# Kernel optimization log

Hardware: AMD Instinct MI355X
Metric: run time of the kernel (lower is better)

Reference implementation:

```python
import jax, jax.numpy as jnp
import numpy as np


def setup_inputs() -> dict:
    key = jax.random.key(0)
    ks = jax.random.split(key, 7)
    N, E, F_in, H = 50000, 800000, 256, 128
    x = jax.random.normal(ks[0], (N, F_in), dtype=jnp.float32)
    edge_index = jax.random.randint(ks[1], (2, E), 0, N, dtype=jnp.int64)
    edge_weight = jax.random.uniform(ks[2], (E,), dtype=jnp.float32)
    W = jax.random.normal(ks[3], (H, F_in), dtype=jnp.float32) * 0.05
    b = jax.random.normal(ks[4], (H,), dtype=jnp.float32) * 0.05
    W_lin = jax.random.normal(ks[5], (2, H), dtype=jnp.float32) * 0.05
    b_lin = jax.random.normal(ks[6], (2,), dtype=jnp.float32) * 0.05
    return {"x": x, "edge_index": edge_index, "edge_weight": edge_weight,
            "W": W, "b": b, "W_lin": W_lin, "b_lin": b_lin}


def reference(x, edge_index, edge_weight, W, b, W_lin, b_lin):
    # GCNConv (PyG semantics): add self-loops (weight 1), symmetric gcn_norm,
    # linear transform, scatter-add aggregation at target, + bias.
    N = x.shape[0]
    loop = jnp.arange(N, dtype=edge_index.dtype)
    src = jnp.concatenate([edge_index[0], loop])  # [E+N]
    dst = jnp.concatenate([edge_index[1], loop])  # [E+N]
    w = jnp.concatenate([edge_weight, jnp.ones((N,), x.dtype)])  # [E+N]
    deg = jax.ops.segment_sum(w, dst, num_segments=N)  # [N]
    dinv = jnp.where(deg > 0, jax.lax.rsqrt(deg), 0.0)
    norm = dinv[src] * w * dinv[dst]  # [E+N]
    xw = x @ W.T  # [N, H] transform-then-gather (fewer FLOPs than gather-then-transform)
    msg = xw[src] * norm[:, None]  # [E+N, H]
    h = jax.ops.segment_sum(msg, dst, num_segments=N) + b  # [N, H]
    # dropout is identity in eval mode
    h = jax.nn.relu(h)
    out = h @ W_lin.T + b_lin  # [N, 2]
    return jax.nn.sigmoid(out)
```

## Files before the change

kernel.cpp:

```cpp
#include <hip/hip_runtime.h>

#define F_IN 256
#define H_DIM 128
#define BIN 64
#define CAP 2048
#define CH 4096

typedef short bf16x8 __attribute__((ext_vector_type(8)));
typedef float f32x4 __attribute__((ext_vector_type(4)));
typedef unsigned short ushort8 __attribute__((ext_vector_type(8)));

__device__ inline unsigned short f2bf(float f) {
    unsigned int u = __float_as_uint(f);
    u += 0x7fffu + ((u >> 16) & 1u);
    return (unsigned short)(u >> 16);
}
__device__ inline float bf_lo(unsigned int u) { return __uint_as_float(u << 16); }
__device__ inline float bf_hi(unsigned int u) { return __uint_as_float(u & 0xffff0000u); }
__device__ inline unsigned int wfx(int wbits) {
    return (unsigned int)__float2uint_rn(__int_as_float(wbits) * 65536.0f);
}

__global__ __launch_bounds__(256) void zero_cur_kernel(int* __restrict__ gcur, int nbins) {
    int i = blockIdx.x * blockDim.x + threadIdx.x;
    if (i < nbins) gcur[i] = 0;
}

__global__ __launch_bounds__(256) void bin_scatter_kernel(const int* __restrict__ ei,
                                                          const float* __restrict__ ew,
                                                          int* __restrict__ gcur,
                                                          int2* __restrict__ binned,
                                                          int E, int nbins) {
    __shared__ unsigned int bh[1024];
    __shared__ int bb[1024];
    __shared__ unsigned int bc[1024];
    int t = threadIdx.x, blk = blockIdx.x;
    for (int i = t; i < 1024; i += 256) { bh[i] = 0; bc[i] = 0; }
    __syncthreads();
    int e0 = blk * CH, e1 = min(e0 + CH, E);
    for (int i = e0 + t; i < e1; i += 256) atomicAdd(&bh[ei[(size_t)E + i] >> 6], 1u);
    __syncthreads();
    for (int b = t; b < nbins; b += 256) {
        int c = (int)bh[b];
        bb[b] = c ? atomicAdd(&gcur[b], c) : 0;
    }
    __syncthreads();
    for (int i = e0 + t; i < e1; i += 256) {
        int s = ei[i];
        int d = ei[(size_t)E + i];
        float wv = ew[i];
        int bin = d >> 6;
        int r = bb[bin] + (int)atomicAdd(&bc[bin], 1u);
        if (r < CAP) {
            int2 p;
            p.x = s | ((d & 63) << 16);
            p.y = __float_as_int(wv);
            binned[(size_t)bin * CAP + r] = p;
        }
    }
}

__global__ __launch_bounds__(256) void gemm_mfma_kernel(const float* __restrict__ x,
                                                        const float* __restrict__ W,
                                                        const int2* __restrict__ binned,
                                                        const int* __restrict__ gcur,
                                                        unsigned short* __restrict__ xs, int N) {
    __shared__ unsigned short As[64 * 64];
    __shared__ unsigned short Bs[128 * 64];
    __shared__ unsigned int fxg[64];
    __shared__ float sdinv[64];
    const int tid = threadIdx.x;
    const int wv = tid >> 6, lane = tid & 63;
    const int block_row = blockIdx.x * 64;

    if (tid < 64) fxg[tid] = 0;
    __syncthreads();
    {
        int ecnt = min(gcur[blockIdx.x], CAP);
        size_t ebase = (size_t)blockIdx.x * CAP;
        for (int i = tid; i < ecnt; i += 256) {
            int2 p = binned[ebase + i];
            atomicAdd(&fxg[(p.x >> 16) & 63], wfx(p.y));
        }
    }
    __syncthreads();
    if (tid < 64) sdinv[tid] = rsqrtf((float)fxg[tid] * (1.0f / 65536.0f) + 1.0f);

    f32x4 acc[8] = {};

    for (int ks = 0; ks < 4; ks++) {
#pragma unroll
        for (int it = 0; it < 2; it++) {
            int gg = it * 256 + tid;
            int row = gg >> 3, g = gg & 7;
            int gr = block_row + row;
            float4 v0 = {0, 0, 0, 0}, v1 = {0, 0, 0, 0};
            if (gr < N) {
                const float4* p = (const float4*)&x[(size_t)gr * F_IN + ks * 64 + g * 8];
                v0 = p[0]; v1 = p[1];
            }
            ushort8 o;
            o[0] = f2bf(v0.x); o[1] = f2bf(v0.y); o[2] = f2bf(v0.z); o[3] = f2bf(v0.w);
            o[4] = f2bf(v1.x); o[5] = f2bf(v1.y); o[6] = f2bf(v1.z); o[7] = f2bf(v1.w);
            int slot = g ^ (row & 7);
            *(ushort8*)&As[row * 64 + slot * 8] = o;
        }
#pragma unroll
        for (int it = 0; it < 4; it++) {
            int gg = it * 256 + tid;
            int col = gg >> 3, g = gg & 7;
            const float4* p = (const float4*)&W[(size_t)col * F_IN + ks * 64 + g * 8];
            float4 v0 = p[0], v1 = p[1];
            ushort8 o;
            o[0] = f2bf(v0.x); o[1] = f2bf(v0.y); o[2] = f2bf(v0.z); o[3] = f2bf(v0.w);
            o[4] = f2bf(v1.x); o[5] = f2bf(v1.y); o[6] = f2bf(v1.z); o[7] = f2bf(v1.w);
            int slot = g ^ (col & 7);
            *(ushort8*)&Bs[col * 64 + slot * 8] = o;
        }
        __syncthreads();
        {
            int lrow = wv * 16 + (lane & 15);
            int lgrp = lane >> 4;
#pragma unroll
            for (int c = 0; c < 2; c++) {
                int sA = (c * 4 + lgrp) ^ (lrow & 7);
                bf16x8 a = *(bf16x8*)&As[lrow * 64 + sA * 8];
#pragma unroll
                for (int j = 0; j < 8; j++) {
                    int col = j * 16 + (lane & 15);
                    int sB = (c * 4 + lgrp) ^ (col & 7);
                    bf16x8 bfr = *(bf16x8*)&Bs[col * 64 + sB * 8];
                    acc[j] = __builtin_amdgcn_mfma_f32_16x16x32_bf16(a, bfr, acc[j], 0, 0, 0);
                }
            }
        }
        __syncthreads();
    }

    const int lc = lane & 15;
#pragma unroll
    for (int j = 0; j < 8; j++) {
#pragma unroll
        for (int r = 0; r < 4; r++) {
            int lrow = wv * 16 + (lane >> 4) * 4 + r;
            int grow = block_row + lrow;
            if (grow < N) {
                float v = acc[j][r] * sdinv[lrow];
                xs[(size_t)grow * H_DIM + j * 16 + lc] = f2bf(v);
            }
        }
    }
}

__global__ __launch_bounds__(512) void bin_gather_kernel(const int2* __restrict__ binned,
                                                         const int* __restrict__ gcur,
                                                         const unsigned int* __restrict__ xs,
                                                         const float* __restrict__ b,
                                                         const float* __restrict__ Wl,
                                                         const float* __restrict__ bl,
                                                         float* __restrict__ out, int N) {
    __shared__ int2 se[CAP];
    __shared__ unsigned int cnt[BIN];
    __shared__ unsigned int fx[BIN];
    __shared__ float sdv[BIN];
    __shared__ int nst[BIN + 1];
    int t = threadIdx.x, blk = blockIdx.x, lane = t & 63, wid = t >> 6;
    int node0 = blk * BIN;
    int ecnt = min(gcur[blk], CAP);
    size_t ebase = (size_t)blk * CAP;

    if (t < BIN) { cnt[t] = 0; fx[t] = 0; }
    __syncthreads();

    int2 eg0 = {0, 0}, eg1 = {0, 0}, eg2 = {0, 0}, eg3 = {0, 0};
#pragma unroll
    for (int k = 0; k < 4; k++) {
        int i = t + k * 512;
        if (i < ecnt) {
            int2 e = binned[ebase + i];
            int dlo = (e.x >> 16) & 63;
            atomicAdd(&cnt[dlo], 1u);
            atomicAdd(&fx[dlo], wfx(e.y));
            if (k == 0) eg0 = e; else if (k == 1) eg1 = e;
            else if (k == 2) eg2 = e; else eg3 = e;
        }
    }
    __syncthreads();
    if (t < BIN) {
        int v = (int)cnt[t];
        int s = v;
#pragma unroll
        for (int off = 1; off < 64; off <<= 1) {
            int tt = __shfl_up(s, off, 64);
            if (lane >= off) s += tt;
        }
        nst[t] = s - v;
        if (t == BIN - 1) nst[BIN] = s;
        sdv[t] = rsqrtf((float)fx[t] * (1.0f / 65536.0f) + 1.0f);
    }
    __syncthreads();
    if (t < BIN) cnt[t] = 0;
    __syncthreads();
#pragma unroll
    for (int k = 0; k < 4; k++) {
        int i = t + k * 512;
        if (i < ecnt) {
            int2 e = (k == 0) ? eg0 : (k == 1) ? eg1 : (k == 2) ? eg2 : eg3;
            int dlo = (e.x >> 16) & 63;
            int r = (int)atomicAdd(&cnt[dlo], 1u);
            int2 o; o.x = e.x & 0xffff; o.y = e.y;
            se[nst[dlo] + r] = o;
        }
    }
    __syncthreads();

    float2 bb2 = ((const float2*)b)[lane];
    float2 wl0 = ((const float2*)Wl)[lane];
    float2 wl1 = ((const float2*)(Wl + H_DIM))[lane];
    float bl0 = bl[0], bl1 = bl[1];
#pragma unroll 1
    for (int i = 0; i < 8; i++) {
        int node = wid * 8 + i;
        int gn = node0 + node;
        if (gn >= N) break;
        int js = nst[node], je = nst[node + 1];
        unsigned int su = xs[(size_t)gn * 64 + lane];
        float ax = bf_lo(su), ay = bf_hi(su);
        int j = js;
        for (; j + 16 <= je; j += 16) {
            int2 q0 = se[j],      q1 = se[j + 1],  q2 = se[j + 2],  q3 = se[j + 3];
            int2 q4 = se[j + 4],  q5 = se[j + 5],  q6 = se[j + 6],  q7 = se[j + 7];
            int2 q8 = se[j + 8],  q9 = se[j + 9],  qa = se[j + 10], qb = se[j + 11];
            int2 qc = se[j + 12], qd = se[j + 13], qe = se[j + 14], qf = se[j + 15];
            unsigned int u0 = xs[(size_t)q0.x * 64 + lane];
            unsigned int u1 = xs[(size_t)q1.x * 64 + lane];
            unsigned int u2 = xs[(size_t)q2.x * 64 + lane];
            unsigned int u3 = xs[(size_t)q3.x * 64 + lane];
            unsigned int u4 = xs[(size_t)q4.x * 64 + lane];
            unsigned int u5 = xs[(size_t)q5.x * 64 + lane];
            unsigned int u6 = xs[(size_t)q6.x * 64 + lane];
            unsigned int u7 = xs[(size_t)q7.x * 64 + lane];
            unsigned int u8 = xs[(size_t)q8.x * 64 + lane];
            unsigned int u9 = xs[(size_t)q9.x * 64 + lane];
            unsigned int ua = xs[(size_t)qa.x * 64 + lane];
            unsigned int ub = xs[(size_t)qb.x * 64 + lane];
            unsigned int uc = xs[(size_t)qc.x * 64 + lane];
            unsigned int ud = xs[(size_t)qd.x * 64 + lane];
            unsigned int ue = xs[(size_t)qe.x * 64 + lane];
            unsigned int uf = xs[(size_t)qf.x * 64 + lane];
            float w0 = __int_as_float(q0.y), w1 = __int_as_float(q1.y);
            float w2 = __int_as_float(q2.y), w3 = __int_as_float(q3.y);
            float w4 = __int_as_float(q4.y), w5 = __int_as_float(q5.y);
            float w6 = __int_as_float(q6.y), w7 = __int_as_float(q7.y);
            float w8 = __int_as_float(q8.y), w9 = __int_as_float(q9.y);
            float wa = __int_as_float(qa.y), wb = __int_as_float(qb.y);
            float wc = __int_as_float(qc.y), wd = __int_as_float(qd.y);
            float we = __int_as_float(qe.y), wf = __int_as_float(qf.y);
            ax += w0 * bf_lo(u0) + w1 * bf_lo(u1) + w2 * bf_lo(u2) + w3 * bf_lo(u3)
                + w4 * bf_lo(u4) + w5 * bf_lo(u5) + w6 * bf_lo(u6) + w7 * bf_lo(u7)
                + w8 * bf_lo(u8) + w9 * bf_lo(u9) + wa * bf_lo(ua) + wb * bf_lo(ub)
                + wc * bf_lo(uc) + wd * bf_lo(ud) + we * bf_lo(ue) + wf * bf_lo(uf);
            ay += w0 * bf_hi(u0) + w1 * bf_hi(u1) + w2 * bf_hi(u2) + w3 * bf_hi(u3)
                + w4 * bf_hi(u4) + w5 * bf_hi(u5) + w6 * bf_hi(u6) + w7 * bf_hi(u7)
                + w8 * bf_hi(u8) + w9 * bf_hi(u9) + wa * bf_hi(ua) + wb * bf_hi(ub)
                + wc * bf_hi(uc) + wd * bf_hi(ud) + we * bf_hi(ue) + wf * bf_hi(uf);
        }
        for (; j + 8 <= je; j += 8) {
            int2 q0 = se[j],     q1 = se[j + 1], q2 = se[j + 2], q3 = se[j + 3];
            int2 q4 = se[j + 4], q5 = se[j + 5], q6 = se[j + 6], q7 = se[j + 7];
            unsigned int u0 = xs[(size_t)q0.x * 64 + lane];
            unsigned int u1 = xs[(size_t)q1.x * 64 + lane];
            unsigned int u2 = xs[(size_t)q2.x * 64 + lane];
            unsigned int u3 = xs[(size_t)q3.x * 64 + lane];
            unsigned int u4 = xs[(size_t)q4.x * 64 + lane];
            unsigned int u5 = xs[(size_t)q5.x * 64 + lane];
            unsigned int u6 = xs[(size_t)q6.x * 64 + lane];
            unsigned int u7 = xs[(size_t)q7.x * 64 + lane];
            float w0 = __int_as_float(q0.y), w1 = __int_as_float(q1.y);
            float w2 = __int_as_float(q2.y), w3 = __int_as_float(q3.y);
            float w4 = __int_as_float(q4.y), w5 = __int_as_float(q5.y);
            float w6 = __int_as_float(q6.y), w7 = __int_as_float(q7.y);
            ax += w0 * bf_lo(u0) + w1 * bf_lo(u1) + w2 * bf_lo(u2) + w3 * bf_lo(u3)
                + w4 * bf_lo(u4) + w5 * bf_lo(u5) + w6 * bf_lo(u6) + w7 * bf_lo(u7);
            ay += w0 * bf_hi(u0) + w1 * bf_hi(u1) + w2 * bf_hi(u2) + w3 * bf_hi(u3)
                + w4 * bf_hi(u4) + w5 * bf_hi(u5) + w6 * bf_hi(u6) + w7 * bf_hi(u7);
        }
        for (; j + 4 <= je; j += 4) {
            int2 q0 = se[j], q1 = se[j + 1], q2 = se[j + 2], q3 = se[j + 3];
            unsigned int u0 = xs[(size_t)q0.x * 64 + lane];
            unsigned int u1 = xs[(size_t)q1.x * 64 + lane];
            unsigned int u2 = xs[(size_t)q2.x * 64 + lane];
            unsigned int u3 = xs[(size_t)q3.x * 64 + lane];
            float w0 = __int_as_float(q0.y), w1 = __int_as_float(q1.y);
            float w2 = __int_as_float(q2.y), w3 = __int_as_float(q3.y);
            ax += w0 * bf_lo(u0) + w1 * bf_lo(u1) + w2 * bf_lo(u2) + w3 * bf_lo(u3);
            ay += w0 * bf_hi(u0) + w1 * bf_hi(u1) + w2 * bf_hi(u2) + w3 * bf_hi(u3);
        }
        for (; j < je; j++) {
            int2 q0 = se[j];
            unsigned int u0 = xs[(size_t)q0.x * 64 + lane];
            float w0 = __int_as_float(q0.y);
            ax += w0 * bf_lo(u0);
            ay += w0 * bf_hi(u0);
        }
        float di = sdv[node];
        float r0 = fmaxf(ax * di + bb2.x, 0.0f);
        float r1 = fmaxf(ay * di + bb2.y, 0.0f);
        float z0 = r0 * wl0.x + r1 * wl0.y;
        float z1 = r0 * wl1.x + r1 * wl1.y;
#pragma unroll
        for (int off = 32; off; off >>= 1) {
            z0 += __shfl_xor(z0, off, 64);
            z1 += __shfl_xor(z1, off, 64);
        }
        if (lane == 0) {
            float2 o;
            o.x = 1.0f / (1.0f + expf(-(z0 + bl0)));
            o.y = 1.0f / (1.0f + expf(-(z1 + bl1)));
            ((float2*)out)[gn] = o;
        }
    }
}

extern "C" void kernel_launch(void* const* d_in, const int* in_sizes, int n_in,
                              void* d_out, int out_size, void* d_ws, size_t ws_size,
                              hipStream_t stream) {
    const float* x  = (const float*)d_in[0];
    const int* ei   = (const int*)d_in[1];
    const float* ew = (const float*)d_in[2];
    const float* W  = (const float*)d_in[3];
    const float* b  = (const float*)d_in[4];
    const float* Wl = (const float*)d_in[5];
    const float* bl = (const float*)d_in[6];
    float* out = (float*)d_out;

    const int N = in_sizes[0] / F_IN;
    const int E = in_sizes[2];
    const int nbins = (N + BIN - 1) / BIN;
    const int nblk  = (E + CH - 1) / CH;

    char* ws = (char*)d_ws;
    size_t off = 0;
    unsigned short* xs = (unsigned short*)(ws + off); off += (size_t)N * H_DIM * 2;
    int2* binned = (int2*)(ws + off); off += (size_t)nbins * CAP * 8;
    int* gcur    = (int*)(ws + off);  off += (size_t)nbins * 4;

    zero_cur_kernel<<<(nbins + 255) / 256, 256, 0, stream>>>(gcur, nbins);
    bin_scatter_kernel<<<nblk, 256, 0, stream>>>(ei, ew, gcur, binned, E, nbins);

    gemm_mfma_kernel<<<nbins, 256, 0, stream>>>(x, W, binned, gcur, xs, N);

    bin_gather_kernel<<<nbins, 512, 0, stream>>>(binned, gcur,
                                                 (const unsigned int*)xs,
                                                 b, Wl, bl, out, N);
}
```

Measured before the change: 98.04 us.

## Halve destination bin size to 32 nodes and shrink gather blocks to 256 threads

Destination bins now cover 32 nodes with capacity 1024 edges, which doubles the bin count. The scatter histograms grow to 2048 entries, and the GEMM kernel still covers 64 rows by reading two bins per block. The gather kernel runs 256-thread blocks with a launch-bounds occupancy hint of 8 and drops the 16-way unrolled edge loop. The aim is more, smaller gather blocks to improve load balance and occupancy, at the cost of more scatter-side atomics and bins, and a capacity of about 1024 per bin that could overflow on dense bins.

Result: faster. 86.19 us (-12.1%).

```diff
diff --git a/kernel.cpp b/kernel.cpp
--- a/kernel.cpp
+++ b/kernel.cpp
@@ -2,8 +2,8 @@
 
 #define F_IN 256
 #define H_DIM 128
-#define BIN 64
-#define CAP 2048
+#define BIN 32
+#define CAP 1024
 #define CH 4096
 
 typedef short bf16x8 __attribute__((ext_vector_type(8)));
@@ -31,14 +31,14 @@
                                                           int* __restrict__ gcur,
                                                           int2* __restrict__ binned,
                                                           int E, int nbins) {
-    __shared__ unsigned int bh[1024];
-    __shared__ int bb[1024];
-    __shared__ unsigned int bc[1024];
+    __shared__ unsigned int bh[2048];
+    __shared__ int bb[2048];
+    __shared__ unsigned int bc[2048];
     int t = threadIdx.x, blk = blockIdx.x;
-    for (int i = t; i < 1024; i += 256) { bh[i] = 0; bc[i] = 0; }
+    for (int i = t; i < 2048; i += 256) { bh[i] = 0; bc[i] = 0; }
     __syncthreads();
     int e0 = blk * CH, e1 = min(e0 + CH, E);
-    for (int i = e0 + t; i < e1; i += 256) atomicAdd(&bh[ei[(size_t)E + i] >> 6], 1u);
+    for (int i = e0 + t; i < e1; i += 256) atomicAdd(&bh[ei[(size_t)E + i] >> 5], 1u);
     __syncthreads();
     for (int b = t; b < nbins; b += 256) {
         int c = (int)bh[b];
@@ -49,11 +49,11 @@
         int s = ei[i];
         int d = ei[(size_t)E + i];
         float wv = ew[i];
-        int bin = d >> 6;
+        int bin = d >> 5;
         int r = bb[bin] + (int)atomicAdd(&bc[bin], 1u);
         if (r < CAP) {
             int2 p;
-            p.x = s | ((d & 63) << 16);
+            p.x = s | ((d & 31) << 16);
             p.y = __float_as_int(wv);
             binned[(size_t)bin * CAP + r] = p;
         }
@@ -64,7 +64,8 @@
                                                         const float* __restrict__ W,
                                                         const int2* __restrict__ binned,
                                                         const int* __restrict__ gcur,
-                                                        unsigned short* __restrict__ xs, int N) {
+                                                        unsigned short* __restrict__ xs,
+                                                        int N, int nbins) {
     __shared__ unsigned short As[64 * 64];
     __shared__ unsigned short Bs[128 * 64];
     __shared__ unsigned int fxg[64];
@@ -75,12 +76,16 @@
 
     if (tid < 64) fxg[tid] = 0;
     __syncthreads();
-    {
-        int ecnt = min(gcur[blockIdx.x], CAP);
-        size_t ebase = (size_t)blockIdx.x * CAP;
-        for (int i = tid; i < ecnt; i += 256) {
-            int2 p = binned[ebase + i];
-            atomicAdd(&fxg[(p.x >> 16) & 63], wfx(p.y));
+#pragma unroll
+    for (int h = 0; h < 2; h++) {
+        int bin = blockIdx.x * 2 + h;
+        if (bin < nbins) {
+            int ecnt = min(gcur[bin], CAP);
+            size_t ebase = (size_t)bin * CAP;
+            for (int i = tid; i < ecnt; i += 256) {
+                int2 p = binned[ebase + i];
+                atomicAdd(&fxg[h * 32 + ((p.x >> 16) & 31)], wfx(p.y));
+            }
         }
     }
     __syncthreads();
@@ -152,13 +157,13 @@
     }
 }
 
-__global__ __launch_bounds__(512) void bin_gather_kernel(const int2* __restrict__ binned,
-                                                         const int* __restrict__ gcur,
-                                                         const unsigned int* __restrict__ xs,
-                                                         const float* __restrict__ b,
-                                                         const float* __restrict__ Wl,
-                                                         const float* __restrict__ bl,
-                                                         float* __restrict__ out, int N) {
+__global__ __launch_bounds__(256, 8) void bin_gather_kernel(const int2* __restrict__ binned,
+                                                            const int* __restrict__ gcur,
+                                                            const unsigned int* __restrict__ xs,
+                                                            const float* __restrict__ b,
+                                                            const float* __restrict__ Wl,
+                                                            const float* __restrict__ bl,
+                                                            float* __restrict__ out, int N) {
     __shared__ int2 se[CAP];
     __shared__ unsigned int cnt[BIN];
     __shared__ unsigned int fx[BIN];
@@ -175,10 +180,10 @@
     int2 eg0 = {0, 0}, eg1 = {0, 0}, eg2 = {0, 0}, eg3 = {0, 0};
 #pragma unroll
     for (int k = 0; k < 4; k++) {
-        int i = t + k * 512;
+        int i = t + k * 256;
         if (i < ecnt) {
             int2 e = binned[ebase + i];
-            int dlo = (e.x >> 16) & 63;
+            int dlo = (e.x >> 16) & 31;
             atomicAdd(&cnt[dlo], 1u);
             atomicAdd(&fx[dlo], wfx(e.y));
             if (k == 0) eg0 = e; else if (k == 1) eg1 = e;
@@ -190,7 +195,7 @@
         int v = (int)cnt[t];
         int s = v;
 #pragma unroll
-        for (int off = 1; off < 64; off <<= 1) {
+        for (int off = 1; off < 32; off <<= 1) {
             int tt = __shfl_up(s, off, 64);
             if (lane >= off) s += tt;
         }
@@ -203,10 +208,10 @@
     __syncthreads();
 #pragma unroll
     for (int k = 0; k < 4; k++) {
-        int i = t + k * 512;
+        int i = t + k * 256;
         if (i < ecnt) {
             int2 e = (k == 0) ? eg0 : (k == 1) ? eg1 : (k == 2) ? eg2 : eg3;
-            int dlo = (e.x >> 16) & 63;
+            int dlo = (e.x >> 16) & 31;
             int r = (int)atomicAdd(&cnt[dlo], 1u);
             int2 o; o.x = e.x & 0xffff; o.y = e.y;
             se[nst[dlo] + r] = o;
@@ -227,44 +232,6 @@
         unsigned int su = xs[(size_t)gn * 64 + lane];
         float ax = bf_lo(su), ay = bf_hi(su);
         int j = js;
-        for (; j + 16 <= je; j += 16) {
-            int2 q0 = se[j],      q1 = se[j + 1],  q2 = se[j + 2],  q3 = se[j + 3];
-            int2 q4 = se[j + 4],  q5 = se[j + 5],  q6 = se[j + 6],  q7 = se[j + 7];
-            int2 q8 = se[j + 8],  q9 = se[j + 9],  qa = se[j + 10], qb = se[j + 11];
-            int2 qc = se[j + 12], qd = se[j + 13], qe = se[j + 14], qf = se[j + 15];
-            unsigned int u0 = xs[(size_t)q0.x * 64 + lane];
-            unsigned int u1 = xs[(size_t)q1.x * 64 + lane];
-            unsigned int u2 = xs[(size_t)q2.x * 64 + lane];
-            unsigned int u3 = xs[(size_t)q3.x * 64 + lane];
-            unsigned int u4 = xs[(size_t)q4.x * 64 + lane];
-            unsigned int u5 = xs[(size_t)q5.x * 64 + lane];
-            unsigned int u6 = xs[(size_t)q6.x * 64 + lane];
-            unsigned int u7 = xs[(size_t)q7.x * 64 + lane];
-            unsigned int u8 = xs[(size_t)q8.x * 64 + lane];
-            unsigned int u9 = xs[(size_t)q9.x * 64 + lane];
-            unsigned int ua = xs[(size_t)qa.x * 64 + lane];
-            unsigned int ub = xs[(size_t)qb.x * 64 + lane];
-            unsigned int uc = xs[(size_t)qc.x * 64 + lane];
-            unsigned int ud = xs[(size_t)qd.x * 64 + lane];
-            unsigned int ue = xs[(size_t)qe.x * 64 + lane];
-            unsigned int uf = xs[(size_t)qf.x * 64 + lane];
-            float w0 = __int_as_float(q0.y), w1 = __int_as_float(q1.y);
-            float w2 = __int_as_float(q2.y), w3 = __int_as_float(q3.y);
-            float w4 = __int_as_float(q4.y), w5 = __int_as_float(q5.y);
-            float w6 = __int_as_float(q6.y), w7 = __int_as_float(q7.y);
-            float w8 = __int_as_float(q8.y), w9 = __int_as_float(q9.y);
-            float wa = __int_as_float(qa.y), wb = __int_as_float(qb.y);
-            float wc = __int_as_float(qc.y), wd = __int_as_float(qd.y);
-            float we = __int_as_float(qe.y), wf = __int_as_float(qf.y);
-            ax += w0 * bf_lo(u0) + w1 * bf_lo(u1) + w2 * bf_lo(u2) + w3 * bf_lo(u3)
-                + w4 * bf_lo(u4) + w5 * bf_lo(u5) + w6 * bf_lo(u6) + w7 * bf_lo(u7)
-                + w8 * bf_lo(u8) + w9 * bf_lo(u9) + wa * bf_lo(ua) + wb * bf_lo(ub)
-                + wc * bf_lo(uc) + wd * bf_lo(ud) + we * bf_lo(ue) + wf * bf_lo(uf);
-            ay += w0 * bf_hi(u0) + w1 * bf_hi(u1) + w2 * bf_hi(u2) + w3 * bf_hi(u3)
-                + w4 * bf_hi(u4) + w5 * bf_hi(u5) + w6 * bf_hi(u6) + w7 * bf_hi(u7)
-                + w8 * bf_hi(u8) + w9 * bf_hi(u9) + wa * bf_hi(ua) + wb * bf_hi(ub)
-                + wc * bf_hi(uc) + wd * bf_hi(ud) + we * bf_hi(ue) + wf * bf_hi(uf);
-        }
         for (; j + 8 <= je; j += 8) {
             int2 q0 = se[j],     q1 = se[j + 1], q2 = se[j + 2], q3 = se[j + 3];
             int2 q4 = se[j + 4], q5 = se[j + 5], q6 = se[j + 6], q7 = se[j + 7];
@@ -348,9 +315,9 @@
     zero_cur_kernel<<<(nbins + 255) / 256, 256, 0, stream>>>(gcur, nbins);
     bin_scatter_kernel<<<nblk, 256, 0, stream>>>(ei, ew, gcur, binned, E, nbins);
 
-    gemm_mfma_kernel<<<nbins, 256, 0, stream>>>(x, W, binned, gcur, xs, N);
-
-    bin_gather_kernel<<<nbins, 512, 0, stream>>>(binned, gcur,
+    gemm_mfma_kernel<<<(N + 63) / 64, 256, 0, stream>>>(x, W, binned, gcur, xs, N, nbins);
+
+    bin_gather_kernel<<<nbins, 256, 0, stream>>>(binned, gcur,
                                                  (const unsigned int*)xs,
                                                  b, Wl, bl, out, N);
 }
```
